# Kernel optimization log

Hardware: AMD Instinct MI355X
Metric: run time of the kernel (lower is better)

## Reference

```python
import jax, jax.numpy as jnp
import numpy as np

K = 32              # neighbors per node (loop=False in knn_graph)
NEG_SLOPE = 0.2     # GATv2Conv default negative_slope


def setup_inputs() -> dict:
    key = jax.random.key(0)
    ks = jax.random.split(key, 5)
    N, D_IN, D_OUT = 10000, 128, 256
    x = jax.random.normal(ks[0], (N, D_IN), dtype=jnp.float32)
    s_in = 1.0 / np.sqrt(D_IN)
    s_out = 1.0 / np.sqrt(D_OUT)
    return {
        "x": x,
        "W_l": jax.random.normal(ks[1], (D_IN, D_OUT), dtype=jnp.float32) * s_in,
        "b_l": jnp.zeros((D_OUT,), dtype=jnp.float32),
        "W_r": jax.random.normal(ks[2], (D_IN, D_OUT), dtype=jnp.float32) * s_in,
        "b_r": jnp.zeros((D_OUT,), dtype=jnp.float32),
        "att": jax.random.normal(ks[3], (D_OUT,), dtype=jnp.float32) * s_out,
        "bias": jnp.zeros((D_OUT,), dtype=jnp.float32),
    }


def _knn_indices(x, k):
    # Squared euclidean cdist, diagonal masked (loop=False), k smallest per row.
    sq = jnp.sum(x * x, axis=1)                       # [N]
    d = sq[:, None] + sq[None, :] - 2.0 * (x @ x.T)   # [N, N]
    d = d + jnp.diag(jnp.full((x.shape[0],), jnp.inf, dtype=x.dtype))
    _, nbr = jax.lax.top_k(-d, k)                     # [N, k] nearest neighbor ids
    return nbr


def reference(x, W_l, b_l, W_r, b_r, att, bias):
    N = x.shape[0]
    nbr = _knn_indices(x, K)                                   # [N, K]
    # GATv2Conv adds self-loops by default -> each node has K+1 sources.
    src = jnp.concatenate([nbr, jnp.arange(N)[:, None]], axis=1)  # [N, K+1]
    h_l = x @ W_l + b_l                                        # source transform [N, D]
    h_r = x @ W_r + b_r                                        # target transform [N, D]
    z = h_l[src] + h_r[:, None, :]                             # [N, K+1, D]
    e = jnp.einsum('nkd,d->nk', jax.nn.leaky_relu(z, NEG_SLOPE), att)  # [N, K+1]
    alpha = jax.nn.softmax(e, axis=1)                          # softmax over sources per target
    out = jnp.einsum('nk,nkd->nd', alpha, h_l[src]) + bias     # [N, D]
    return out
```

## Files before the change

kernel.cpp:

```cpp
#include <hip/hip_runtime.h>
#include <hip/hip_fp16.h>

#define NN     10000
#define DI     128
#define DO     256
#define KNB    32
#define NSRC   33
#define RB     16
#define NP2    10240
#define NTILE  640
#define ATILE  626
#define NCB    20
#define SEG    64
#define CAP    1024
#define NEG    0.2f

typedef __attribute__((ext_vector_type(8))) short bf16x8;
typedef __attribute__((ext_vector_type(4))) float f32x4;

__device__ __forceinline__ unsigned fkey(float f) {
    unsigned u = __float_as_uint(f);
    return (u & 0x80000000u) ? ~u : (u | 0x80000000u);
}
__device__ __forceinline__ unsigned short bf16rne(float f) {
    unsigned u = __float_as_uint(f);
    unsigned r = u + 0x7FFFu + ((u >> 16) & 1u);
    return (unsigned short)(r >> 16);
}

__global__ __launch_bounds__(256) void prep_k(const float* __restrict__ x,
    unsigned short* __restrict__ Bh, double* __restrict__ sq64,
    float* __restrict__ sq32)
{
    __shared__ float xs[16][132];
    const int t = threadIdx.x;
    const int tile = blockIdx.x;
    const int i0 = tile * 16;
#pragma unroll
    for (int q = 0; q < 2; ++q) {
        const int idx = t + 256 * q;
        const int r = idx >> 5, c4 = idx & 31;
        float4 v = make_float4(0.f, 0.f, 0.f, 0.f);
        if (i0 + r < NN) v = *(const float4*)(x + (size_t)(i0 + r) * DI + c4 * 4);
        *(float4*)&xs[r][c4 * 4] = v;
    }
    __syncthreads();
    const int ks = t >> 6, flane = t & 63;
    const int srow = flane & 15;
    const int kb = ks * 32 + ((flane >> 4) & 3) * 8;
    unsigned hi2[4];
#pragma unroll
    for (int j = 0; j < 4; ++j) {
        const float v0 = xs[srow][kb + 2 * j], v1 = xs[srow][kb + 2 * j + 1];
        hi2[j] = (unsigned)bf16rne(v0) | ((unsigned)bf16rne(v1) << 16);
    }
    *(uint4*)(Bh + ((size_t)(tile * 4 + ks) * 64 + flane) * 8) =
        make_uint4(hi2[0], hi2[1], hi2[2], hi2[3]);
    const int row = t >> 4, sub = t & 15;
    double s = 0.0;
#pragma unroll
    for (int q = 0; q < 8; ++q) {
        const float v = xs[row][sub * 8 + q];
        s = fma((double)v, (double)v, s);
    }
#pragma unroll
    for (int off = 8; off >= 1; off >>= 1) s += __shfl_xor(s, off);
    if (sub == 0) {
        const int gi = i0 + row;
        sq32[gi] = (gi < NN) ? (float)s : 0.f;
        if (gi < ATILE * 16) sq64[gi] = s;
    }
}

__global__ __launch_bounds__(256) void thresh_k(
    const unsigned short* __restrict__ Bh, const float* __restrict__ sq32,
    unsigned* __restrict__ Trow)
{
    __shared__ unsigned short dist16[RB][512];
    const int rt = blockIdx.x;
    const int r0 = rt * 16;
    const int t = threadIdx.x;
    const int wid = t >> 6, lane = t & 63;
    const int wbase = wid * 128, l15 = lane & 15, rgrp = (lane >> 4) * 4;

    bf16x8 ah[4];
#pragma unroll
    for (int ks = 0; ks < 4; ++ks)
        ah[ks] = *(const bf16x8*)(Bh + ((size_t)(rt * 4 + ks) * 64 + lane) * 8);
    float sqiv[4];
#pragma unroll
    for (int rg = 0; rg < 4; ++rg) sqiv[rg] = sq32[r0 + rgrp + rg];

#pragma unroll 1
    for (int ct = 0; ct < 8; ++ct) {
        const int ctg = wid * 8 + ct;
        bf16x8 bh[4];
#pragma unroll
        for (int ks = 0; ks < 4; ++ks)
            bh[ks] = *(const bf16x8*)(Bh + ((size_t)(ctg * 4 + ks) * 64 + lane) * 8);
        f32x4 acc = {0.f, 0.f, 0.f, 0.f};
#pragma unroll
        for (int ks = 0; ks < 4; ++ks)
            acc = __builtin_amdgcn_mfma_f32_16x16x32_bf16(ah[ks], bh[ks], acc, 0, 0, 0);
        const int col = wbase + ct * 16 + l15;
        const float sqj = sq32[col];
#pragma unroll
        for (int rg = 0; rg < 4; ++rg) {
            const int row = r0 + rgrp + rg;
            const float dd = __builtin_fmaf(-2.f, acc[rg], sqiv[rg] + sqj);
            unsigned k16 = (__float_as_uint(dd) >> 16) | 0x8000u;
            if (col >= NN || col == row) k16 = 0xFFFFu;
            dist16[rgrp + rg][col] = (unsigned short)k16;
        }
    }
    __syncthreads();

#pragma unroll 1
    for (int rr = 0; rr < 4; ++rr) {
        const int r = wid * 4 + rr;
        unsigned kk[8];
#pragma unroll
        for (int u = 0; u < 8; ++u) kk[u] = dist16[r][lane + 64 * u];
        unsigned lo = 0, hi = 0xFFFFu;
#pragma unroll 1
        for (int it = 0; it < 16; ++it) {
            const unsigned mid = (lo + hi) >> 1;
            int c2 = 0;
#pragma unroll
            for (int u = 0; u < 8; ++u)
                c2 += (int)__popcll(__ballot(kk[u] <= mid));
            if (c2 >= 16) hi = mid; else lo = mid;
        }
        if (lane == 0) Trow[r0 + r] = ((hi & 0x7FFFu) << 16) | 0xFFFFu;
    }
}

__global__ __launch_bounds__(256) void knn_emit_k(
    const unsigned short* __restrict__ Bh, const float* __restrict__ sq32,
    const unsigned* __restrict__ Trow, unsigned* __restrict__ cnt,
    unsigned* __restrict__ cand)
{
    __shared__ unsigned lcnt[32];
    __shared__ unsigned basebuf[32];
    __shared__ unsigned cbuf[32][SEG];
    const int r0 = blockIdx.x * 32;
    const int cbase = blockIdx.y * 512;
    const int t = threadIdx.x;
    const int wid = t >> 6, lane = t & 63;
    const int wbase = wid * 128, l15 = lane & 15, rgrp = (lane >> 4) * 4;
    if (t < 32) lcnt[t] = 0;

    bf16x8 ah[2][4];
#pragma unroll
    for (int rt2 = 0; rt2 < 2; ++rt2)
#pragma unroll
        for (int ks = 0; ks < 4; ++ks) {
            const int rt = (r0 >> 4) + rt2;
            ah[rt2][ks] = *(const bf16x8*)(Bh + ((size_t)(rt * 4 + ks) * 64 + lane) * 8);
        }
    float sqiv[2][4];
    unsigned TUv[2][4];
#pragma unroll
    for (int rt2 = 0; rt2 < 2; ++rt2)
#pragma unroll
        for (int rg = 0; rg < 4; ++rg) {
            const int row = r0 + rt2 * 16 + rgrp + rg;
            sqiv[rt2][rg] = sq32[row];
            TUv[rt2][rg] = Trow[row];
        }
    float sqjv[8];
#pragma unroll
    for (int ct = 0; ct < 8; ++ct)
        sqjv[ct] = sq32[cbase + wbase + ct * 16 + l15];
    __syncthreads();

    const int ctg0 = (cbase >> 4) + wid * 8;
    bf16x8 bh[4];
#pragma unroll
    for (int ks = 0; ks < 4; ++ks)
        bh[ks] = *(const bf16x8*)(Bh + ((size_t)(ctg0 * 4 + ks) * 64 + lane) * 8);

#pragma unroll 1
    for (int ct = 0; ct < 8; ++ct) {
        bf16x8 bhn[4];
        if (ct < 7) {
#pragma unroll
            for (int ks = 0; ks < 4; ++ks)
                bhn[ks] = *(const bf16x8*)(Bh + ((size_t)((ctg0 + ct + 1) * 4 + ks) * 64 + lane) * 8);
        }
        f32x4 a0 = {0.f, 0.f, 0.f, 0.f}, a1 = {0.f, 0.f, 0.f, 0.f};
#pragma unroll
        for (int ks = 0; ks < 4; ++ks) {
            a0 = __builtin_amdgcn_mfma_f32_16x16x32_bf16(ah[0][ks], bh[ks], a0, 0, 0, 0);
            a1 = __builtin_amdgcn_mfma_f32_16x16x32_bf16(ah[1][ks], bh[ks], a1, 0, 0, 0);
        }
        const int col = cbase + wbase + ct * 16 + l15;
        const float sqj = sqjv[ct];
#pragma unroll
        for (int rt2 = 0; rt2 < 2; ++rt2)
#pragma unroll
            for (int rg = 0; rg < 4; ++rg) {
                const int lrow = rt2 * 16 + rgrp + rg;
                const float dd = __builtin_fmaf(-2.f, (rt2 ? a1 : a0)[rg],
                                                sqiv[rt2][rg] + sqj);
                const unsigned raw = __float_as_uint(dd);
                if ((raw <= TUv[rt2][rg]) && (col < NN) && (col != r0 + lrow)) {
                    const unsigned slot = atomicAdd(&lcnt[lrow], 1u);
                    if (slot < SEG)
                        cbuf[lrow][slot] =
                            (((raw >> 16) | 0x8000u) << 16) | (unsigned)col;
                }
            }
#pragma unroll
        for (int ks = 0; ks < 4; ++ks) bh[ks] = bhn[ks];
    }

    __syncthreads();
    if (t < 32) {
        unsigned c = lcnt[t]; if (c > SEG) c = SEG;
        lcnt[t] = c;
        basebuf[t] = atomicAdd(&cnt[r0 + t], c);
    }
    __syncthreads();
#pragma unroll
    for (int q = 0; q < (32 * SEG) / 256; ++q) {
        const int idx = t + 256 * q;
        const int lr = idx >> 6, sl = idx & 63;
        if ((unsigned)sl < lcnt[lr]) {
            const unsigned b = basebuf[lr] + (unsigned)sl;
            if (b < CAP) cand[(size_t)(r0 + lr) * CAP + b] = cbuf[lr][sl];
        }
    }
}

__global__ __launch_bounds__(256) void rerank_select_k(
    const float* __restrict__ x, const double* __restrict__ sq64,
    const unsigned* __restrict__ cand, const unsigned* __restrict__ cnt,
    int* __restrict__ nbr)
{
    __shared__ unsigned cbuf[64];
    __shared__ float xrs[DI];
    __shared__ unsigned long long kbuf[64];
    const int i = blockIdx.x, t = threadIdx.x;
    const int lane = t & 63;

    if (t >= 64 && t < 96)
        *(float4*)&xrs[(t - 64) * 4] = *(const float4*)(x + (size_t)i * DI + (t - 64) * 4);

    if (t < 64) {
        cbuf[lane] = 0xFFFFFFFFu;
        unsigned n = cnt[i]; if (n > CAP) n = CAP;
        unsigned kk[CAP / 64];
#pragma unroll
        for (int u = 0; u < CAP / 64; ++u) {
            const unsigned idx = (unsigned)lane + 64u * u;
            kk[u] = (idx < n) ? cand[(size_t)i * CAP + idx] : 0xFFFFFFFFu;
        }
        unsigned lo = 0, hi = 0xFFFFFFFFu;
#pragma unroll 1
        for (int it = 0; it < 32; ++it) {
            const unsigned mid = lo + ((hi - lo) >> 1);
            int c2 = 0;
#pragma unroll
            for (int u = 0; u < CAP / 64; ++u)
                c2 += (int)__popcll(__ballot(kk[u] <= mid));
            if (c2 >= 64) hi = mid; else lo = mid;
        }
        const unsigned T = hi;
        const unsigned long long lml = (1ull << lane) - 1;
        unsigned pref = 0;
#pragma unroll
        for (int u = 0; u < CAP / 64; ++u) {
            const unsigned long long b = __ballot(kk[u] <= T);
            const int slot = (int)pref + (int)__popcll(b & lml);
            if (kk[u] <= T && slot < 64) cbuf[slot] = kk[u];
            pref += (unsigned)__popcll(b);
        }
    }
    __syncthreads();

    const unsigned c32 = cbuf[t >> 2];
    const int col = (int)(c32 & 0xFFFFu);
    const bool valid = (col < NN);
    const int sc = valid ? col : 0;
    const int sub = t & 3;
    double a = 0.0;
    const float* xc = x + (size_t)sc * DI + sub * 32;
    const float* xr = &xrs[sub * 32];
#pragma unroll
    for (int q = 0; q < 8; ++q) {
        const float4 v = *(const float4*)(xc + q * 4);
        const float4 r = *(const float4*)(xr + q * 4);
        a = fma((double)r.x, (double)v.x, a);
        a = fma((double)r.y, (double)v.y, a);
        a = fma((double)r.z, (double)v.z, a);
        a = fma((double)r.w, (double)v.w, a);
    }
    a += __shfl_xor(a, 1);
    a += __shfl_xor(a, 2);
    if (sub == 0) {
        const float dd = (float)(sq64[i] + sq64[sc] - 2.0 * a);
        kbuf[t >> 2] = valid
            ? (((unsigned long long)fkey(dd) << 32) | (unsigned)col) : ~0ull;
    }
    __syncthreads();

    if (t < 64) {
        const unsigned long long key = kbuf[lane];
        int rank = 0;
#pragma unroll 1
        for (int l = 0; l < 64; ++l) {
            const unsigned long long kl = __shfl(key, l);
            rank += (kl < key) ? 1 : 0;
        }
        if (key != ~0ull && rank < KNB) nbr[(size_t)i * KNB + rank] = (int)(key & 0xFFFFu);
    }
}

__global__ __launch_bounds__(256) void hgemm_k(
    const float* __restrict__ x, const float* __restrict__ Wl,
    const float* __restrict__ bl, const float* __restrict__ Wr,
    const float* __restrict__ br, __half* __restrict__ hl16, float* __restrict__ hr)
{
    const int c = threadIdx.x;
    const int r0 = blockIdx.x * RB;
    float accl[RB], accr[RB];
    const float blv = bl[c], brv = br[c];
#pragma unroll
    for (int r = 0; r < RB; ++r) { accl[r] = blv; accr[r] = brv; }
    for (int d = 0; d < DI; ++d) {
        const float wl = Wl[d * DO + c];
        const float wr = Wr[d * DO + c];
#pragma unroll
        for (int r = 0; r < RB; ++r) {
            const float xv = x[(size_t)(r0 + r) * DI + d];
            accl[r] = fmaf(xv, wl, accl[r]);
            accr[r] = fmaf(xv, wr, accr[r]);
        }
    }
#pragma unroll
    for (int r = 0; r < RB; ++r) {
        hl16[(size_t)(r0 + r) * DO + c] = __float2half(accl[r]);
        hr[(size_t)(r0 + r) * DO + c] = accr[r];
    }
}

__global__ __launch_bounds__(256) void gat_k(
    const __half* __restrict__ hl16, const float* __restrict__ hr,
    const int* __restrict__ nbr, const float* __restrict__ att,
    const float* __restrict__ bias, float* __restrict__ out)
{
    __shared__ int src[NSRC];
    __shared__ __align__(16) __half hbuf[NSRC][DO];
    __shared__ float eS[NSRC];
    __shared__ float alphaS[NSRC];
    const int i = blockIdx.x, t = threadIdx.x;
    if (t < KNB) src[t] = nbr[(size_t)i * KNB + t];
    if (t == KNB) src[KNB] = i;
    __syncthreads();

    {
        const int sub = t & 31, rb = t >> 5;
#pragma unroll
        for (int s = 0; s < 5; ++s) {
            const int rk = s * 8 + rb;
            if (rk < NSRC)
                *(uint4*)&hbuf[rk][sub * 8] =
                    *(const uint4*)(hl16 + (size_t)src[rk] * DO + sub * 8);
        }
    }
    __syncthreads();

    const int wid = t >> 6, lane = t & 63;
    {
        const float4 hr4 = *(const float4*)(hr + (size_t)i * DO + lane * 4);
        const float4 at4 = *(const float4*)(att + lane * 4);
#pragma unroll 1
        for (int k = wid; k < NSRC; k += 4) {
            const __half2 h01 = *(const __half2*)&hbuf[k][lane * 4];
            const __half2 h23 = *(const __half2*)&hbuf[k][lane * 4 + 2];
            const float2 f01 = __half22float2(h01);
            const float2 f23 = __half22float2(h23);
            float z, p = 0.f;
            z = f01.x + hr4.x; p = fmaf(z > 0.f ? z : NEG * z, at4.x, p);
            z = f01.y + hr4.y; p = fmaf(z > 0.f ? z : NEG * z, at4.y, p);
            z = f23.x + hr4.z; p = fmaf(z > 0.f ? z : NEG * z, at4.z, p);
            z = f23.y + hr4.w; p = fmaf(z > 0.f ? z : NEG * z, at4.w, p);
#pragma unroll
            for (int off = 32; off >= 1; off >>= 1) p += __shfl_xor(p, off);
            if (lane == 0) eS[k] = p;
        }
    }
    __syncthreads();
    if (wid == 0) {
        const float v = (lane < NSRC) ? eS[lane] : -3.4e38f;
        float m = v;
#pragma unroll
        for (int off = 32; off >= 1; off >>= 1) m = fmaxf(m, __shfl_xor(m, off));
        float w = (lane < NSRC) ? __expf(v - m) : 0.f;
        float s = w;
#pragma unroll
        for (int off = 32; off >= 1; off >>= 1) s += __shfl_xor(s, off);
        if (lane < NSRC) alphaS[lane] = w / s;
    }
    __syncthreads();
    float o = bias[t];
#pragma unroll
    for (int k = 0; k < NSRC; ++k)
        o = fmaf(alphaS[k], __half2float(hbuf[k][t]), o);
    out[(size_t)i * DO + t] = o;
}

extern "C" void kernel_launch(void* const* d_in, const int* in_sizes, int n_in,
                              void* d_out, int out_size, void* d_ws, size_t ws_size,
                              hipStream_t stream) {
    const float* x    = (const float*)d_in[0];
    const float* Wl   = (const float*)d_in[1];
    const float* bl   = (const float*)d_in[2];
    const float* Wr   = (const float*)d_in[3];
    const float* br   = (const float*)d_in[4];
    const float* att  = (const float*)d_in[5];
    const float* bias = (const float*)d_in[6];
    float* out = (float*)d_out;

    char* ws = (char*)d_ws;
    unsigned short* Bh  = (unsigned short*)(ws + 0);
    double* sq64 = (double*)(ws + 2621440);
    float*  sq32 = (float*)(ws + 2701568);
    unsigned* Trow = (unsigned*)(ws + 2742528);
    unsigned* cnt  = (unsigned*)(ws + 2782592);
    int*    nbr  = (int*)(ws + 2822656);
    unsigned* cand = (unsigned*)(ws + 4102656);
    __half* hl16 = (__half*)(ws + 4102656);
    float*  hr   = (float*)(ws + 9222656);

    hipMemsetAsync(cnt, 0, ATILE * 16 * sizeof(unsigned), stream);
    prep_k<<<dim3(NTILE), 256, 0, stream>>>(x, Bh, sq64, sq32);
    thresh_k<<<dim3(ATILE), 256, 0, stream>>>(Bh, sq32, Trow);
    knn_emit_k<<<dim3(ATILE / 2, NCB), 256, 0, stream>>>(Bh, sq32, Trow, cnt, cand);
    rerank_select_k<<<dim3(NN), 256, 0, stream>>>(x, sq64, cand, cnt, nbr);
    hgemm_k<<<dim3(NN / RB), 256, 0, stream>>>(x, Wl, bl, Wr, br, hl16, hr);
    gat_k<<<dim3(NN), 256, 0, stream>>>(hl16, hr, nbr, att, bias, out);
}
```

Measured before the change: 259.4 us.

## Fold cnt memset into prep kernel and process four rows per rerank block

Removes the separate memset launch by zeroing the candidate counters inside prep_k. Reworks rerank_select_k so each 64-lane wavefront handles one row (four rows per block) instead of one row per 256-thread block. The threshold search now bisects only the upper 16 bits of each candidate key, which cuts the iteration count in half. To absorb the coarser threshold it keeps up to 128 candidates and has each lane compute two full-length fp64 dot products. Ranking reads keys from shared memory, and more candidates per row raises the rerank arithmetic while the coarser threshold may admit more ties.

```diff
diff --git a/kernel.cpp b/kernel.cpp
--- a/kernel.cpp
+++ b/kernel.cpp
@@ -13,6 +13,7 @@
 #define NCB    20
 #define SEG    64
 #define CAP    1024
+#define RCAND  128
 #define NEG    0.2f
 
 typedef __attribute__((ext_vector_type(8))) short bf16x8;
@@ -30,12 +31,16 @@
 
 __global__ __launch_bounds__(256) void prep_k(const float* __restrict__ x,
     unsigned short* __restrict__ Bh, double* __restrict__ sq64,
-    float* __restrict__ sq32)
+    float* __restrict__ sq32, unsigned* __restrict__ cnt)
 {
     __shared__ float xs[16][132];
     const int t = threadIdx.x;
     const int tile = blockIdx.x;
     const int i0 = tile * 16;
+    if (tile < 40) {
+        const int idx = tile * 256 + t;
+        if (idx < ATILE * 16) cnt[idx] = 0;
+    }
 #pragma unroll
     for (int q = 0; q < 2; ++q) {
         const int idx = t + 256 * q;
@@ -238,83 +243,91 @@
     const unsigned* __restrict__ cand, const unsigned* __restrict__ cnt,
     int* __restrict__ nbr)
 {
-    __shared__ unsigned cbuf[64];
-    __shared__ float xrs[DI];
-    __shared__ unsigned long long kbuf[64];
-    const int i = blockIdx.x, t = threadIdx.x;
-    const int lane = t & 63;
-
-    if (t >= 64 && t < 96)
-        *(float4*)&xrs[(t - 64) * 4] = *(const float4*)(x + (size_t)i * DI + (t - 64) * 4);
-
-    if (t < 64) {
-        cbuf[lane] = 0xFFFFFFFFu;
-        unsigned n = cnt[i]; if (n > CAP) n = CAP;
-        unsigned kk[CAP / 64];
-#pragma unroll
-        for (int u = 0; u < CAP / 64; ++u) {
-            const unsigned idx = (unsigned)lane + 64u * u;
-            kk[u] = (idx < n) ? cand[(size_t)i * CAP + idx] : 0xFFFFFFFFu;
-        }
-        unsigned lo = 0, hi = 0xFFFFFFFFu;
-#pragma unroll 1
-        for (int it = 0; it < 32; ++it) {
-            const unsigned mid = lo + ((hi - lo) >> 1);
-            int c2 = 0;
-#pragma unroll
-            for (int u = 0; u < CAP / 64; ++u)
-                c2 += (int)__popcll(__ballot(kk[u] <= mid));
-            if (c2 >= 64) hi = mid; else lo = mid;
-        }
-        const unsigned T = hi;
-        const unsigned long long lml = (1ull << lane) - 1;
-        unsigned pref = 0;
-#pragma unroll
-        for (int u = 0; u < CAP / 64; ++u) {
-            const unsigned long long b = __ballot(kk[u] <= T);
-            const int slot = (int)pref + (int)__popcll(b & lml);
-            if (kk[u] <= T && slot < 64) cbuf[slot] = kk[u];
-            pref += (unsigned)__popcll(b);
-        }
-    }
-    __syncthreads();
-
-    const unsigned c32 = cbuf[t >> 2];
-    const int col = (int)(c32 & 0xFFFFu);
-    const bool valid = (col < NN);
-    const int sc = valid ? col : 0;
-    const int sub = t & 3;
-    double a = 0.0;
-    const float* xc = x + (size_t)sc * DI + sub * 32;
-    const float* xr = &xrs[sub * 32];
-#pragma unroll
-    for (int q = 0; q < 8; ++q) {
-        const float4 v = *(const float4*)(xc + q * 4);
-        const float4 r = *(const float4*)(xr + q * 4);
-        a = fma((double)r.x, (double)v.x, a);
-        a = fma((double)r.y, (double)v.y, a);
-        a = fma((double)r.z, (double)v.z, a);
-        a = fma((double)r.w, (double)v.w, a);
-    }
-    a += __shfl_xor(a, 1);
-    a += __shfl_xor(a, 2);
-    if (sub == 0) {
-        const float dd = (float)(sq64[i] + sq64[sc] - 2.0 * a);
-        kbuf[t >> 2] = valid
-            ? (((unsigned long long)fkey(dd) << 32) | (unsigned)col) : ~0ull;
-    }
-    __syncthreads();
-
-    if (t < 64) {
-        const unsigned long long key = kbuf[lane];
-        int rank = 0;
-#pragma unroll 1
-        for (int l = 0; l < 64; ++l) {
-            const unsigned long long kl = __shfl(key, l);
-            rank += (kl < key) ? 1 : 0;
-        }
-        if (key != ~0ull && rank < KNB) nbr[(size_t)i * KNB + rank] = (int)(key & 0xFFFFu);
-    }
+    __shared__ float xrs[4][DI];
+    __shared__ unsigned cbuf[4][RCAND];
+    __shared__ unsigned long long kbuf[4][RCAND];
+    const int t = threadIdx.x;
+    const int w = t >> 6, lane = t & 63;
+    const int i = blockIdx.x * 4 + w;
+
+    cbuf[w][lane] = 0xFFFFFFFFu;
+    cbuf[w][lane + 64] = 0xFFFFFFFFu;
+    if (lane < 32)
+        *(float4*)&xrs[w][lane * 4] = *(const float4*)(x + (size_t)i * DI + lane * 4);
+
+    unsigned n = cnt[i]; if (n > CAP) n = CAP;
+    unsigned kk[CAP / 64];
+#pragma unroll
+    for (int u = 0; u < CAP / 64; ++u) {
+        const unsigned idx = (unsigned)lane + 64u * u;
+        kk[u] = (idx < n) ? cand[(size_t)i * CAP + idx] : 0xFFFFFFFFu;
+    }
+    unsigned lo = 0, hi = 0xFFFFu;
+#pragma unroll 1
+    for (int it = 0; it < 16; ++it) {
+        const unsigned mid = (lo + hi) >> 1;
+        int c2 = 0;
+#pragma unroll
+        for (int u = 0; u < CAP / 64; ++u)
+            c2 += (int)__popcll(__ballot((kk[u] >> 16) <= mid));
+        if (c2 >= 64) hi = mid; else lo = mid;
+    }
+    const unsigned T = hi;
+    const unsigned long long lml = (1ull << lane) - 1;
+    unsigned pref = 0;
+#pragma unroll
+    for (int u = 0; u < CAP / 64; ++u) {
+        const bool pass = (kk[u] >> 16) <= T;
+        const unsigned long long b = __ballot(pass);
+        const int slot = (int)pref + (int)__popcll(b & lml);
+        if (pass && slot < RCAND) cbuf[w][slot] = kk[u];
+        pref += (unsigned)__popcll(b);
+    }
+    __syncthreads();
+
+    const unsigned cA = cbuf[w][2 * lane], cB = cbuf[w][2 * lane + 1];
+    const int colA = (int)(cA & 0xFFFFu), colB = (int)(cB & 0xFFFFu);
+    const bool vA = colA < NN, vB = colB < NN;
+    const float* xa = x + (size_t)(vA ? colA : 0) * DI;
+    const float* xb = x + (size_t)(vB ? colB : 0) * DI;
+    double aA = 0.0, aB = 0.0;
+#pragma unroll 4
+    for (int q = 0; q < 32; ++q) {
+        const float4 fa = *(const float4*)(xa + q * 4);
+        const float4 fb = *(const float4*)(xb + q * 4);
+        const float4 fr = *(const float4*)(&xrs[w][q * 4]);
+        aA = fma((double)fr.x, (double)fa.x, aA);
+        aA = fma((double)fr.y, (double)fa.y, aA);
+        aA = fma((double)fr.z, (double)fa.z, aA);
+        aA = fma((double)fr.w, (double)fa.w, aA);
+        aB = fma((double)fr.x, (double)fb.x, aB);
+        aB = fma((double)fr.y, (double)fb.y, aB);
+        aB = fma((double)fr.z, (double)fb.z, aB);
+        aB = fma((double)fr.w, (double)fb.w, aB);
+    }
+    const double sqi = sq64[i];
+    unsigned long long keyA = ~0ull, keyB = ~0ull;
+    if (vA) {
+        const float dd = (float)(sqi + sq64[colA] - 2.0 * aA);
+        keyA = ((unsigned long long)fkey(dd) << 32) | (unsigned)colA;
+    }
+    if (vB) {
+        const float dd = (float)(sqi + sq64[colB] - 2.0 * aB);
+        keyB = ((unsigned long long)fkey(dd) << 32) | (unsigned)colB;
+    }
+    kbuf[w][2 * lane] = keyA;
+    kbuf[w][2 * lane + 1] = keyB;
+    __syncthreads();
+
+    int rA = 0, rB = 0;
+#pragma unroll 8
+    for (int j = 0; j < RCAND; ++j) {
+        const unsigned long long kj = kbuf[w][j];
+        rA += (kj < keyA) ? 1 : 0;
+        rB += (kj < keyB) ? 1 : 0;
+    }
+    if (vA && rA < KNB) nbr[(size_t)i * KNB + rA] = colA;
+    if (vB && rB < KNB) nbr[(size_t)i * KNB + rB] = colB;
 }
 
 __global__ __launch_bounds__(256) void hgemm_k(
@@ -434,11 +447,10 @@
     __half* hl16 = (__half*)(ws + 4102656);
     float*  hr   = (float*)(ws + 9222656);
 
-    hipMemsetAsync(cnt, 0, ATILE * 16 * sizeof(unsigned), stream);
-    prep_k<<<dim3(NTILE), 256, 0, stream>>>(x, Bh, sq64, sq32);
+    prep_k<<<dim3(NTILE), 256, 0, stream>>>(x, Bh, sq64, sq32, cnt);
     thresh_k<<<dim3(ATILE), 256, 0, stream>>>(Bh, sq32, Trow);
     knn_emit_k<<<dim3(ATILE / 2, NCB), 256, 0, stream>>>(Bh, sq32, Trow, cnt, cand);
-    rerank_select_k<<<dim3(NN), 256, 0, stream>>>(x, sq64, cand, cnt, nbr);
+    rerank_select_k<<<dim3(NN / 4), 256, 0, stream>>>(x, sq64, cand, cnt, nbr);
     hgemm_k<<<dim3(NN / RB), 256, 0, stream>>>(x, Wl, bl, Wr, br, hl16, hr);
     gat_k<<<dim3(NN), 256, 0, stream>>>(hl16, hr, nbr, att, bias, out);
 }
```

After: 269.6 us. 1.04x slower.

## Replace bisection candidate select with two-level radix histogram and fold memset into prep

Applied to the files above, without the earlier changes.

The rerank kernel previously ran a 32-step ballot bisection over up to 1024 candidates on a single wavefront to find the 64 smallest approximate keys. It now builds two 256-bin shared-memory histograms over the top 16 key bits using all 256 threads, and keeps every candidate at or below the 16-bit threshold, up to 128, for exact fp64 reranking. The final rank is computed over 128 keys read from shared memory. The separate hipMemsetAsync for the counters is folded into prep_k, removing one launch. The risks are extra rerank work on 128 candidates, and overflow past 128 when many keys share the threshold bin, which could drop true neighbours.

```diff
diff --git a/kernel.cpp b/kernel.cpp
--- a/kernel.cpp
+++ b/kernel.cpp
@@ -13,6 +13,7 @@
 #define NCB    20
 #define SEG    64
 #define CAP    1024
+#define RCAND  128
 #define NEG    0.2f
 
 typedef __attribute__((ext_vector_type(8))) short bf16x8;
@@ -30,12 +31,16 @@
 
 __global__ __launch_bounds__(256) void prep_k(const float* __restrict__ x,
     unsigned short* __restrict__ Bh, double* __restrict__ sq64,
-    float* __restrict__ sq32)
+    float* __restrict__ sq32, unsigned* __restrict__ cnt)
 {
     __shared__ float xs[16][132];
     const int t = threadIdx.x;
     const int tile = blockIdx.x;
     const int i0 = tile * 16;
+    if (tile < 40) {
+        const int idx = tile * 256 + t;
+        if (idx < ATILE * 16) cnt[idx] = 0;
+    }
 #pragma unroll
     for (int q = 0; q < 2; ++q) {
         const int idx = t + 256 * q;
@@ -238,82 +243,144 @@
     const unsigned* __restrict__ cand, const unsigned* __restrict__ cnt,
     int* __restrict__ nbr)
 {
-    __shared__ unsigned cbuf[64];
+    __shared__ unsigned hist[256];
+    __shared__ unsigned hist2[256];
     __shared__ float xrs[DI];
-    __shared__ unsigned long long kbuf[64];
+    __shared__ unsigned cbuf[RCAND];
+    __shared__ unsigned long long kbuf[RCAND];
+    __shared__ unsigned sel[4];
     const int i = blockIdx.x, t = threadIdx.x;
     const int lane = t & 63;
 
-    if (t >= 64 && t < 96)
-        *(float4*)&xrs[(t - 64) * 4] = *(const float4*)(x + (size_t)i * DI + (t - 64) * 4);
-
+    hist[t] = 0; hist2[t] = 0;
+    if (t < RCAND) cbuf[t] = 0xFFFFFFFFu;
+    if (t >= 128 && t < 160)
+        *(float4*)&xrs[(t - 128) * 4] =
+            *(const float4*)(x + (size_t)i * DI + (t - 128) * 4);
+    if (t == 0) { sel[0] = 0xFFFFFFFFu; sel[2] = 0xFFFFu; sel[3] = 0; }
+    unsigned n = cnt[i]; if (n > CAP) n = CAP;
+    unsigned kk[4];
+#pragma unroll
+    for (int u = 0; u < 4; ++u) {
+        const unsigned idx = (unsigned)t + 256u * u;
+        kk[u] = (idx < n) ? cand[(size_t)i * CAP + idx] : 0xFFFFFFFFu;
+    }
+    __syncthreads();
+
+#pragma unroll
+    for (int u = 0; u < 4; ++u)
+        if (kk[u] != 0xFFFFFFFFu) atomicAdd(&hist[kk[u] >> 24], 1u);
+    __syncthreads();
     if (t < 64) {
-        cbuf[lane] = 0xFFFFFFFFu;
-        unsigned n = cnt[i]; if (n > CAP) n = CAP;
-        unsigned kk[CAP / 64];
-#pragma unroll
-        for (int u = 0; u < CAP / 64; ++u) {
-            const unsigned idx = (unsigned)lane + 64u * u;
-            kk[u] = (idx < n) ? cand[(size_t)i * CAP + idx] : 0xFFFFFFFFu;
-        }
-        unsigned lo = 0, hi = 0xFFFFFFFFu;
-#pragma unroll 1
-        for (int it = 0; it < 32; ++it) {
-            const unsigned mid = lo + ((hi - lo) >> 1);
-            int c2 = 0;
-#pragma unroll
-            for (int u = 0; u < CAP / 64; ++u)
-                c2 += (int)__popcll(__ballot(kk[u] <= mid));
-            if (c2 >= 64) hi = mid; else lo = mid;
-        }
-        const unsigned T = hi;
+        unsigned h[4];
+#pragma unroll
+        for (int q = 0; q < 4; ++q) h[q] = hist[lane * 4 + q];
+        const unsigned s = h[0] + h[1] + h[2] + h[3];
+        unsigned pre = s;
+#pragma unroll
+        for (int off = 1; off < 64; off <<= 1) {
+            const unsigned o = __shfl_up(pre, off);
+            if (lane >= off) pre += o;
+        }
+        const unsigned B = pre - s;
+        if (B < 64 && B + s >= 64) {
+            unsigned c = B, H = 0, rr = 0;
+#pragma unroll
+            for (int q = 0; q < 4; ++q) {
+                if (c < 64 && c + h[q] >= 64) { H = lane * 4 + q; rr = 64 - c; break; }
+                c += h[q];
+            }
+            sel[0] = H; sel[1] = rr;
+        }
+    }
+    __syncthreads();
+    const unsigned H = sel[0];
+
+    if (H != 0xFFFFFFFFu) {
+#pragma unroll
+        for (int u = 0; u < 4; ++u)
+            if (kk[u] != 0xFFFFFFFFu && (kk[u] >> 24) == H)
+                atomicAdd(&hist2[(kk[u] >> 16) & 0xFFu], 1u);
+    }
+    __syncthreads();
+    if (t < 64 && H != 0xFFFFFFFFu) {
+        const unsigned r = sel[1];
+        unsigned h[4];
+#pragma unroll
+        for (int q = 0; q < 4; ++q) h[q] = hist2[lane * 4 + q];
+        const unsigned s = h[0] + h[1] + h[2] + h[3];
+        unsigned pre = s;
+#pragma unroll
+        for (int off = 1; off < 64; off <<= 1) {
+            const unsigned o = __shfl_up(pre, off);
+            if (lane >= off) pre += o;
+        }
+        const unsigned B = pre - s;
+        if (B < r && B + s >= r) {
+            unsigned c = B, L = 0;
+#pragma unroll
+            for (int q = 0; q < 4; ++q) {
+                if (c < r && c + h[q] >= r) { L = lane * 4 + q; break; }
+                c += h[q];
+            }
+            sel[2] = (H << 8) | L;
+        }
+    }
+    __syncthreads();
+    const unsigned T16 = sel[2];
+
+    {
         const unsigned long long lml = (1ull << lane) - 1;
-        unsigned pref = 0;
-#pragma unroll
-        for (int u = 0; u < CAP / 64; ++u) {
-            const unsigned long long b = __ballot(kk[u] <= T);
-            const int slot = (int)pref + (int)__popcll(b & lml);
-            if (kk[u] <= T && slot < 64) cbuf[slot] = kk[u];
-            pref += (unsigned)__popcll(b);
-        }
-    }
-    __syncthreads();
-
-    const unsigned c32 = cbuf[t >> 2];
-    const int col = (int)(c32 & 0xFFFFu);
-    const bool valid = (col < NN);
-    const int sc = valid ? col : 0;
-    const int sub = t & 3;
+#pragma unroll
+        for (int u = 0; u < 4; ++u) {
+            const bool pass = (kk[u] != 0xFFFFFFFFu) && ((kk[u] >> 16) <= T16);
+            const unsigned long long b = __ballot(pass);
+            unsigned base = 0;
+            if (lane == 0 && b) base = atomicAdd(&sel[3], (unsigned)__popcll(b));
+            base = __shfl(base, 0);
+            if (pass) {
+                const int slot = (int)(base + (unsigned)__popcll(b & lml));
+                if (slot < RCAND) cbuf[slot] = kk[u];
+            }
+        }
+    }
+    __syncthreads();
+
+    const int c = t >> 1, h = t & 1;
+    const unsigned cc = cbuf[c];
+    const int col = (int)(cc & 0xFFFFu);
+    const bool valid = col < NN;
+    const float* xc = x + (size_t)(valid ? col : 0) * DI;
     double a = 0.0;
-    const float* xc = x + (size_t)sc * DI + sub * 32;
-    const float* xr = &xrs[sub * 32];
-#pragma unroll
-    for (int q = 0; q < 8; ++q) {
-        const float4 v = *(const float4*)(xc + q * 4);
-        const float4 r = *(const float4*)(xr + q * 4);
-        a = fma((double)r.x, (double)v.x, a);
-        a = fma((double)r.y, (double)v.y, a);
-        a = fma((double)r.z, (double)v.z, a);
-        a = fma((double)r.w, (double)v.w, a);
+#pragma unroll
+    for (int q = 0; q < 16; ++q) {
+        const int fi = q * 8 + h * 4;
+        const float4 v = *(const float4*)(xc + fi);
+        const float4 r4 = *(const float4*)(&xrs[fi]);
+        a = fma((double)r4.x, (double)v.x, a);
+        a = fma((double)r4.y, (double)v.y, a);
+        a = fma((double)r4.z, (double)v.z, a);
+        a = fma((double)r4.w, (double)v.w, a);
     }
     a += __shfl_xor(a, 1);
-    a += __shfl_xor(a, 2);
-    if (sub == 0) {
-        const float dd = (float)(sq64[i] + sq64[sc] - 2.0 * a);
-        kbuf[t >> 2] = valid
-            ? (((unsigned long long)fkey(dd) << 32) | (unsigned)col) : ~0ull;
-    }
-    __syncthreads();
-
-    if (t < 64) {
-        const unsigned long long key = kbuf[lane];
+    if (h == 0) {
+        unsigned long long key = ~0ull;
+        if (valid) {
+            const float dd = (float)(sq64[i] + sq64[col] - 2.0 * a);
+            key = ((unsigned long long)fkey(dd) << 32) | (unsigned)col;
+        }
+        kbuf[c] = key;
+    }
+    __syncthreads();
+
+    if (t < RCAND) {
+        const unsigned long long key = kbuf[t];
         int rank = 0;
-#pragma unroll 1
-        for (int l = 0; l < 64; ++l) {
-            const unsigned long long kl = __shfl(key, l);
-            rank += (kl < key) ? 1 : 0;
-        }
-        if (key != ~0ull && rank < KNB) nbr[(size_t)i * KNB + rank] = (int)(key & 0xFFFFu);
+#pragma unroll 8
+        for (int j = 0; j < RCAND; ++j)
+            rank += (kbuf[j] < key) ? 1 : 0;
+        if (key != ~0ull && rank < KNB)
+            nbr[(size_t)i * KNB + rank] = (int)(key & 0xFFFFu);
     }
 }
 
@@ -434,8 +501,7 @@
     __half* hl16 = (__half*)(ws + 4102656);
     float*  hr   = (float*)(ws + 9222656);
 
-    hipMemsetAsync(cnt, 0, ATILE * 16 * sizeof(unsigned), stream);
-    prep_k<<<dim3(NTILE), 256, 0, stream>>>(x, Bh, sq64, sq32);
+    prep_k<<<dim3(NTILE), 256, 0, stream>>>(x, Bh, sq64, sq32, cnt);
     thresh_k<<<dim3(ATILE), 256, 0, stream>>>(Bh, sq32, Trow);
     knn_emit_k<<<dim3(ATILE / 2, NCB), 256, 0, stream>>>(Bh, sq32, Trow, cnt, cand);
     rerank_select_k<<<dim3(NN), 256, 0, stream>>>(x, sq64, cand, cnt, nbr);
```

Measured after the change: 235.4 us. 1.1x faster.
